# Kernel tuning notes

Hardware: AMD Instinct MI355X
Metric: run time of the kernel (lower is better)

Reference implementation:

```python
import jax, jax.numpy as jnp
import numpy as np

EPSILON = 1e-30

def compute_energy_density(F, lam, mu):
    # F: [E,3,3]; lam, mu: [E]
    C = jnp.einsum('...ji,...jk->...ik', F, F)
    J = jnp.linalg.det(F)
    Ic = C[..., 0, 0] + C[..., 1, 1] + C[..., 2, 2]
    delta = 1.0
    dim = 3
    alpha = (1.0 - 1.0 / (dim + delta)) * mu / lam + 1.0
    Ic_verified = jax.nn.relu(Ic + delta)
    return (mu / 2 * (Ic - dim)
            + lam / 2 * (J - alpha) ** 2
            - 0.5 * mu * jnp.log(Ic_verified + EPSILON))


def setup_inputs() -> dict:
    key = jax.random.key(0)
    ks = jax.random.split(key, 10)
    V, E = 8192, 40000
    next_position = jax.random.normal(ks[0], (V, 3), dtype=jnp.float32)
    position = jax.random.normal(ks[1], (V, 3), dtype=jnp.float32)
    velocity = jax.random.normal(ks[2], (V, 3), dtype=jnp.float32) * 0.1
    external_acceleration = jax.random.normal(ks[3], (V, 3), dtype=jnp.float32) * 0.1
    int_density_matrix = jax.random.uniform(ks[4], (V, V), dtype=jnp.float32)
    elements = jax.random.randint(ks[5], (E, 4), 0, V, dtype=jnp.int64)
    polynomials = jax.random.normal(ks[6], (E, 4, 4), dtype=jnp.float32)
    measure = jax.random.uniform(ks[7], (E, 4, 1), dtype=jnp.float32)
    lam = jax.random.uniform(ks[8], (E,), dtype=jnp.float32) + 1.0  # keep away from 0 (divided by in alpha)
    mu = jax.random.uniform(ks[9], (E,), dtype=jnp.float32) + 0.5
    time_step = jnp.ones((), dtype=jnp.float32)
    return {"next_position": next_position, "position": position, "velocity": velocity,
            "external_acceleration": external_acceleration, "int_density_matrix": int_density_matrix,
            "elements": elements, "polynomials": polynomials, "measure": measure,
            "lam": lam, "mu": mu, "time_step": time_step}


def reference(next_position, position, velocity, external_acceleration,
              int_density_matrix, elements, polynomials, measure, lam, mu, time_step):
    inv_h = 1.0 / time_step
    coefficient = inv_h ** 2 / 2
    # Kinetic term: einsum('ij,ji->', M, delta @ delta.T) == sum(delta * (M @ delta))
    # (avoids materializing the [V,V] delta @ delta.T intermediate)
    y = position + velocity * time_step + external_acceleration * time_step ** 2
    delta = next_position - y  # [V,3]
    kinetic_energy = coefficient * jnp.sum(delta * (int_density_matrix @ delta))
    # Elastic term: gather element vertex positions, build deformation gradient F
    basis_derivatives_q = polynomials[:, :4, :3]          # [E,4,3]
    local_position = next_position[elements]               # [E,4,3] gather
    F = jnp.einsum('bft,bfl->btl', local_position, basis_derivatives_q)  # [E,3,3]
    psi = compute_energy_density(F, lam, mu)               # [E]
    elastic_energy = jnp.einsum('b,b->', psi, measure[:, 3, 0])
    energy = kinetic_energy + elastic_energy
    return energy, kinetic_energy, elastic_energy
```

## Files before the change

kernel.cpp:

```cpp
#include <hip/hip_runtime.h>

#define V 8192
#define RPW 2
#define KBLOCKS (V / (RPW * 4))

__global__ __launch_bounds__(256) void prep_kernel(
    const float* __restrict__ next_pos, const float* __restrict__ pos,
    const float* __restrict__ vel, const float* __restrict__ ext,
    const float* __restrict__ dt_p, float* __restrict__ ws) {
  int i = blockIdx.x * blockDim.x + threadIdx.x;
  if (i < 2) ws[i] = 0.f;
  if (i < V) {
    float dt = dt_p[0];
    float dt2 = dt * dt;
    float* dx = ws + 16;
    float* dy = dx + V;
    float* dz = dy + V;
    dx[i] = next_pos[3*i+0] - (pos[3*i+0] + vel[3*i+0]*dt + ext[3*i+0]*dt2);
    dy[i] = next_pos[3*i+1] - (pos[3*i+1] + vel[3*i+1]*dt + ext[3*i+1]*dt2);
    dz[i] = next_pos[3*i+2] - (pos[3*i+2] + vel[3*i+2]*dt + ext[3*i+2]*dt2);
  }
}

__global__ __launch_bounds__(256) void kinetic_kernel(
    const float* __restrict__ M, const float* __restrict__ dsoa,
    float* __restrict__ acc) {
  const float* __restrict__ dx = dsoa;
  const float* __restrict__ dy = dsoa + V;
  const float* __restrict__ dz = dsoa + 2 * V;
  const float4* __restrict__ dx4 = (const float4*)dx;
  const float4* __restrict__ dy4 = (const float4*)dy;
  const float4* __restrict__ dz4 = (const float4*)dz;

  const int t = threadIdx.x;
  const int lane = t & 63;
  const int wv = t >> 6;
  const int wave = blockIdx.x * 4 + wv;
  const int r0 = wave * RPW;

  float rx[RPW], ry[RPW], rz[RPW];
#pragma unroll
  for (int r = 0; r < RPW; ++r) {
    rx[r] = dx[r0 + r];
    ry[r] = dy[r0 + r];
    rz[r] = dz[r0 + r];
  }

  float a = 0.f;
#pragma unroll 2
  for (int i = 0; i < V / 4 / 64; ++i) {
    const int k = i * 64 + lane;
    const float4 cx = dx4[k];
    const float4 cy = dy4[k];
    const float4 cz = dz4[k];
#pragma unroll
    for (int r = 0; r < RPW; ++r) {
      const float4 m = *(const float4*)(M + (size_t)(r0 + r) * V + 4 * k);
      a += m.x * (rx[r]*cx.x + ry[r]*cy.x + rz[r]*cz.x);
      a += m.y * (rx[r]*cx.y + ry[r]*cy.y + rz[r]*cz.y);
      a += m.z * (rx[r]*cx.z + ry[r]*cy.z + rz[r]*cz.z);
      a += m.w * (rx[r]*cx.w + ry[r]*cy.w + rz[r]*cz.w);
    }
  }

#pragma unroll
  for (int off = 32; off; off >>= 1) a += __shfl_down(a, off, 64);

  __shared__ float lds[4];
  if (lane == 0) lds[wv] = a;
  __syncthreads();
  if (t == 0) atomicAdd(acc, lds[0] + lds[1] + lds[2] + lds[3]);
}

__global__ __launch_bounds__(256) void elastic_kernel(
    const float* __restrict__ next_pos, const int* __restrict__ elements,
    const float* __restrict__ poly, const float* __restrict__ measure,
    const float* __restrict__ lam, const float* __restrict__ mu,
    float* __restrict__ acc, int E) {
  int e = blockIdx.x * blockDim.x + threadIdx.x;
  float contrib = 0.f;
  if (e < E) {
    float F00 = 0.f, F01 = 0.f, F02 = 0.f;
    float F10 = 0.f, F11 = 0.f, F12 = 0.f;
    float F20 = 0.f, F21 = 0.f, F22 = 0.f;
#pragma unroll
    for (int f = 0; f < 4; ++f) {
      int vi = elements[e * 4 + f];
      const float* p = next_pos + 3 * (size_t)vi;
      float px = p[0], py = p[1], pz = p[2];
      const float* b = poly + (size_t)e * 16 + f * 4;
      float b0 = b[0], b1 = b[1], b2 = b[2];
      F00 += px * b0; F01 += px * b1; F02 += px * b2;
      F10 += py * b0; F11 += py * b1; F12 += py * b2;
      F20 += pz * b0; F21 += pz * b1; F22 += pz * b2;
    }
    float Ic = F00*F00 + F01*F01 + F02*F02 +
               F10*F10 + F11*F11 + F12*F12 +
               F20*F20 + F21*F21 + F22*F22;
    float J = F00 * (F11 * F22 - F12 * F21)
            - F01 * (F10 * F22 - F12 * F20)
            + F02 * (F10 * F21 - F11 * F20);
    float l = lam[e], m = mu[e];
    float alpha = 0.75f * m / l + 1.f;
    float Icv = fmaxf(Ic + 1.f, 0.f);
    float d = J - alpha;
    float psi = 0.5f * m * (Ic - 3.f) + 0.5f * l * d * d
              - 0.5f * m * logf(Icv + 1e-30f);
    contrib = psi * measure[e * 4 + 3];
  }
#pragma unroll
  for (int off = 32; off; off >>= 1) contrib += __shfl_down(contrib, off, 64);
  __shared__ float w[4];
  int lane = threadIdx.x & 63, wv = threadIdx.x >> 6;
  if (lane == 0) w[wv] = contrib;
  __syncthreads();
  if (threadIdx.x == 0) atomicAdd(acc, w[0] + w[1] + w[2] + w[3]);
}

__global__ void finalize_kernel(const float* __restrict__ ws,
                                const float* __restrict__ dt_p,
                                float* __restrict__ out) {
  float dt = dt_p[0];
  float inv_h = 1.f / dt;
  float coeff = 0.5f * inv_h * inv_h;
  float kin = coeff * ws[0];
  float ela = ws[1];
  out[0] = kin + ela;
  out[1] = kin;
  out[2] = ela;
}

extern "C" void kernel_launch(void* const* d_in, const int* in_sizes, int n_in,
                              void* d_out, int out_size, void* d_ws, size_t ws_size,
                              hipStream_t stream) {
  const float* next_pos = (const float*)d_in[0];
  const float* pos      = (const float*)d_in[1];
  const float* vel      = (const float*)d_in[2];
  const float* ext      = (const float*)d_in[3];
  const float* M        = (const float*)d_in[4];
  const int*   elements = (const int*)d_in[5];
  const float* poly     = (const float*)d_in[6];
  const float* measure  = (const float*)d_in[7];
  const float* lam      = (const float*)d_in[8];
  const float* mu       = (const float*)d_in[9];
  const float* dt_p     = (const float*)d_in[10];
  float* out = (float*)d_out;
  float* ws  = (float*)d_ws;
  const int E = in_sizes[5] / 4;

  prep_kernel<<<(V + 255) / 256, 256, 0, stream>>>(next_pos, pos, vel, ext, dt_p, ws);
  kinetic_kernel<<<KBLOCKS, 256, 0, stream>>>(M, ws + 16, ws);
  elastic_kernel<<<(E + 255) / 256, 256, 0, stream>>>(next_pos, elements, poly,
                                                      measure, lam, mu, ws + 1, E);
  finalize_kernel<<<1, 1, 0, stream>>>(ws, dt_p, out);
}
```

Before: 388.5 us.

## Stage delta vectors in LDS tiles and batch M row loads per wave

The kinetic kernel now gives each wave a single row of M instead of two, which doubles the grid. The block cooperatively loads 1024-element tiles of the delta vectors into shared memory, so the vectors are no longer re-read from global or L2 by every wave. Each lane issues four float4 loads of M up front per tile to increase memory-level parallelism. In exchange the kernel adds two barriers per tile, halves per-wave work, and re-reads the vectors once per block, in a kernel that streams 256MB of M and is bandwidth-bound.

```diff
diff --git a/kernel.cpp b/kernel.cpp
--- a/kernel.cpp
+++ b/kernel.cpp
@@ -1,8 +1,10 @@
 #include <hip/hip_runtime.h>
 
 #define V 8192
-#define RPW 2
-#define KBLOCKS (V / (RPW * 4))
+#define TILE 1024
+#define NTILES (V / TILE)
+#define C4_PER_TILE (TILE / 4)
+#define ITERS (C4_PER_TILE / 64)
 
 __global__ __launch_bounds__(256) void prep_kernel(
     const float* __restrict__ next_pos, const float* __restrict__ pos,
@@ -25,51 +27,58 @@
 __global__ __launch_bounds__(256) void kinetic_kernel(
     const float* __restrict__ M, const float* __restrict__ dsoa,
     float* __restrict__ acc) {
-  const float* __restrict__ dx = dsoa;
-  const float* __restrict__ dy = dsoa + V;
-  const float* __restrict__ dz = dsoa + 2 * V;
-  const float4* __restrict__ dx4 = (const float4*)dx;
-  const float4* __restrict__ dy4 = (const float4*)dy;
-  const float4* __restrict__ dz4 = (const float4*)dz;
+  const float4* __restrict__ dx4 = (const float4*)dsoa;
+  const float4* __restrict__ dy4 = (const float4*)(dsoa + V);
+  const float4* __restrict__ dz4 = (const float4*)(dsoa + 2 * V);
+
+  __shared__ float4 lx[C4_PER_TILE], ly[C4_PER_TILE], lz[C4_PER_TILE];
+  __shared__ float wsum[4];
 
   const int t = threadIdx.x;
   const int lane = t & 63;
   const int wv = t >> 6;
-  const int wave = blockIdx.x * 4 + wv;
-  const int r0 = wave * RPW;
+  const int row = blockIdx.x * 4 + wv;
 
-  float rx[RPW], ry[RPW], rz[RPW];
-#pragma unroll
-  for (int r = 0; r < RPW; ++r) {
-    rx[r] = dx[r0 + r];
-    ry[r] = dy[r0 + r];
-    rz[r] = dz[r0 + r];
-  }
+  const float rx = ((const float*)dx4)[row];
+  const float ry = ((const float*)dy4)[row];
+  const float rz = ((const float*)dz4)[row];
+
+  const float4* __restrict__ Mrow4 = (const float4*)(M + (size_t)row * V);
 
   float a = 0.f;
-#pragma unroll 2
-  for (int i = 0; i < V / 4 / 64; ++i) {
-    const int k = i * 64 + lane;
-    const float4 cx = dx4[k];
-    const float4 cy = dy4[k];
-    const float4 cz = dz4[k];
+  for (int tl = 0; tl < NTILES; ++tl) {
+    const int g = tl * C4_PER_TILE + t;
+    lx[t] = dx4[g];
+    ly[t] = dy4[g];
+    lz[t] = dz4[g];
+    __syncthreads();
+
+    float4 mv[ITERS];
 #pragma unroll
-    for (int r = 0; r < RPW; ++r) {
-      const float4 m = *(const float4*)(M + (size_t)(r0 + r) * V + 4 * k);
-      a += m.x * (rx[r]*cx.x + ry[r]*cy.x + rz[r]*cz.x);
-      a += m.y * (rx[r]*cx.y + ry[r]*cy.y + rz[r]*cz.y);
-      a += m.z * (rx[r]*cx.z + ry[r]*cy.z + rz[r]*cz.z);
-      a += m.w * (rx[r]*cx.w + ry[r]*cy.w + rz[r]*cz.w);
+    for (int j = 0; j < ITERS; ++j)
+      mv[j] = Mrow4[tl * C4_PER_TILE + j * 64 + lane];
+
+#pragma unroll
+    for (int j = 0; j < ITERS; ++j) {
+      const int c = j * 64 + lane;
+      const float4 cx = lx[c];
+      const float4 cy = ly[c];
+      const float4 cz = lz[c];
+      const float4 m = mv[j];
+      a += m.x * (rx * cx.x + ry * cy.x + rz * cz.x);
+      a += m.y * (rx * cx.y + ry * cy.y + rz * cz.y);
+      a += m.z * (rx * cx.z + ry * cy.z + rz * cz.z);
+      a += m.w * (rx * cx.w + ry * cy.w + rz * cz.w);
     }
+    __syncthreads();
   }
 
 #pragma unroll
   for (int off = 32; off; off >>= 1) a += __shfl_down(a, off, 64);
 
-  __shared__ float lds[4];
-  if (lane == 0) lds[wv] = a;
+  if (lane == 0) wsum[wv] = a;
   __syncthreads();
-  if (t == 0) atomicAdd(acc, lds[0] + lds[1] + lds[2] + lds[3]);
+  if (t == 0) atomicAdd(acc, wsum[0] + wsum[1] + wsum[2] + wsum[3]);
 }
 
 __global__ __launch_bounds__(256) void elastic_kernel(
@@ -149,7 +158,7 @@
   const int E = in_sizes[5] / 4;
 
   prep_kernel<<<(V + 255) / 256, 256, 0, stream>>>(next_pos, pos, vel, ext, dt_p, ws);
-  kinetic_kernel<<<KBLOCKS, 256, 0, stream>>>(M, ws + 16, ws);
+  kinetic_kernel<<<V / 4, 256, 0, stream>>>(M, ws + 16, ws);
   elastic_kernel<<<(E + 255) / 256, 256, 0, stream>>>(next_pos, elements, poly,
                                                       measure, lam, mu, ws + 1, E);
   finalize_kernel<<<1, 1, 0, stream>>>(ws, dt_p, out);
```

New measurement: 411.3 us. 1.06x slower.

## Fuse prep with elastic, grid-stride kinetic GEMV, last-block finalize

Applied to the files above, without the earlier changes.

Merges the delta-prep and elastic-energy kernels into one launch, using block-index ranges to pick the role. The kinetic kernel now walks M as a flat float4 stream with a grid-stride pattern, each thread keeping one fixed column chunk of delta and re-reading row deltas from cache. The separate finalize kernel is replaced by a last-block-done atomic counter. This cuts launch count from four to two and aims for fully coalesced streaming of the 256MB matrix, at the cost of an extra atomic ticket and more scalar loads per iteration.

```diff
diff --git a/kernel.cpp b/kernel.cpp
--- a/kernel.cpp
+++ b/kernel.cpp
@@ -1,133 +1,154 @@
 #include <hip/hip_runtime.h>
 
 #define V 8192
-#define RPW 2
-#define KBLOCKS (V / (RPW * 4))
+#define PREP_BLOCKS 32
+#define KIN_BLOCKS 2048
+#define KIN_THREADS 256
+#define KIN_TOTAL (KIN_BLOCKS * KIN_THREADS)
 
-__global__ __launch_bounds__(256) void prep_kernel(
+
+__global__ __launch_bounds__(256) void prep_elastic_kernel(
     const float* __restrict__ next_pos, const float* __restrict__ pos,
     const float* __restrict__ vel, const float* __restrict__ ext,
-    const float* __restrict__ dt_p, float* __restrict__ ws) {
-  int i = blockIdx.x * blockDim.x + threadIdx.x;
-  if (i < 2) ws[i] = 0.f;
-  if (i < V) {
-    float dt = dt_p[0];
-    float dt2 = dt * dt;
+    const float* __restrict__ dt_p, const int* __restrict__ elements,
+    const float* __restrict__ poly, const float* __restrict__ measure,
+    const float* __restrict__ lam, const float* __restrict__ mu,
+    float* __restrict__ ws, int E) {
+  const int b = blockIdx.x;
+  const int t = threadIdx.x;
+
+  if (b < PREP_BLOCKS) {
+    if (b == 0 && t == 0) {
+      ws[0] = 0.f;
+      ((unsigned int*)ws)[2] = 0u;
+    }
+    const int i = b * 256 + t;
+    const float dt = dt_p[0];
+    const float dt2 = dt * dt;
     float* dx = ws + 16;
     float* dy = dx + V;
     float* dz = dy + V;
     dx[i] = next_pos[3*i+0] - (pos[3*i+0] + vel[3*i+0]*dt + ext[3*i+0]*dt2);
     dy[i] = next_pos[3*i+1] - (pos[3*i+1] + vel[3*i+1]*dt + ext[3*i+1]*dt2);
     dz[i] = next_pos[3*i+2] - (pos[3*i+2] + vel[3*i+2]*dt + ext[3*i+2]*dt2);
+  } else {
+    const int e = (b - PREP_BLOCKS) * 256 + t;
+    float contrib = 0.f;
+    if (e < E) {
+      float F00 = 0.f, F01 = 0.f, F02 = 0.f;
+      float F10 = 0.f, F11 = 0.f, F12 = 0.f;
+      float F20 = 0.f, F21 = 0.f, F22 = 0.f;
+#pragma unroll
+      for (int f = 0; f < 4; ++f) {
+        int vi = elements[e * 4 + f];
+        const float* p = next_pos + 3 * (size_t)vi;
+        float px = p[0], py = p[1], pz = p[2];
+        const float* bd = poly + (size_t)e * 16 + f * 4;
+        float b0 = bd[0], b1 = bd[1], b2 = bd[2];
+        F00 += px * b0; F01 += px * b1; F02 += px * b2;
+        F10 += py * b0; F11 += py * b1; F12 += py * b2;
+        F20 += pz * b0; F21 += pz * b1; F22 += pz * b2;
+      }
+      float Ic = F00*F00 + F01*F01 + F02*F02 +
+                 F10*F10 + F11*F11 + F12*F12 +
+                 F20*F20 + F21*F21 + F22*F22;
+      float J = F00 * (F11 * F22 - F12 * F21)
+              - F01 * (F10 * F22 - F12 * F20)
+              + F02 * (F10 * F21 - F11 * F20);
+      float l = lam[e], m = mu[e];
+      float alpha = 0.75f * m / l + 1.f;
+      float Icv = fmaxf(Ic + 1.f, 0.f);
+      float d = J - alpha;
+      float psi = 0.5f * m * (Ic - 3.f) + 0.5f * l * d * d
+                - 0.5f * m * logf(Icv + 1e-30f);
+      contrib = psi * measure[e * 4 + 3];
+    }
+#pragma unroll
+    for (int off = 32; off; off >>= 1) contrib += __shfl_down(contrib, off, 64);
+    __shared__ float w[4];
+    int lane = t & 63, wv = t >> 6;
+    if (lane == 0) w[wv] = contrib;
+    __syncthreads();
+    if (t == 0) atomicAdd(ws + 1, w[0] + w[1] + w[2] + w[3]);
   }
 }
 
-__global__ __launch_bounds__(256) void kinetic_kernel(
-    const float* __restrict__ M, const float* __restrict__ dsoa,
-    float* __restrict__ acc) {
-  const float* __restrict__ dx = dsoa;
-  const float* __restrict__ dy = dsoa + V;
-  const float* __restrict__ dz = dsoa + 2 * V;
-  const float4* __restrict__ dx4 = (const float4*)dx;
-  const float4* __restrict__ dy4 = (const float4*)dy;
-  const float4* __restrict__ dz4 = (const float4*)dz;
+__global__ __launch_bounds__(KIN_THREADS) void kinetic_kernel(
+    const float* __restrict__ M, float* __restrict__ ws,
+    const float* __restrict__ dt_p, float* __restrict__ out) {
+  const float* __restrict__ dsoa = ws + 16;
+  const float* __restrict__ dxs = dsoa;
+  const float* __restrict__ dys = dsoa + V;
+  const float* __restrict__ dzs = dsoa + 2 * V;
 
   const int t = threadIdx.x;
-  const int lane = t & 63;
-  const int wv = t >> 6;
-  const int wave = blockIdx.x * 4 + wv;
-  const int r0 = wave * RPW;
+  const unsigned base = blockIdx.x * KIN_THREADS + t;
 
-  float rx[RPW], ry[RPW], rz[RPW];
-#pragma unroll
-  for (int r = 0; r < RPW; ++r) {
-    rx[r] = dx[r0 + r];
-    ry[r] = dy[r0 + r];
-    rz[r] = dz[r0 + r];
-  }
+  const unsigned c = base & 2047u;
+  const float4 cx = ((const float4*)dxs)[c];
+  const float4 cy = ((const float4*)dys)[c];
+  const float4 cz = ((const float4*)dzs)[c];
+
+  const float4* __restrict__ M4 = (const float4*)M;
 
   float a = 0.f;
-#pragma unroll 2
-  for (int i = 0; i < V / 4 / 64; ++i) {
-    const int k = i * 64 + lane;
-    const float4 cx = dx4[k];
-    const float4 cy = dy4[k];
-    const float4 cz = dz4[k];
-#pragma unroll
-    for (int r = 0; r < RPW; ++r) {
-      const float4 m = *(const float4*)(M + (size_t)(r0 + r) * V + 4 * k);
-      a += m.x * (rx[r]*cx.x + ry[r]*cy.x + rz[r]*cz.x);
-      a += m.y * (rx[r]*cx.y + ry[r]*cy.y + rz[r]*cz.y);
-      a += m.z * (rx[r]*cx.z + ry[r]*cy.z + rz[r]*cz.z);
-      a += m.w * (rx[r]*cx.w + ry[r]*cy.w + rz[r]*cz.w);
-    }
+  const int NIT = (V / 4) * V / KIN_TOTAL;
+#pragma unroll 1
+  for (int it = 0; it < NIT; it += 4) {
+    unsigned g0 = base + (unsigned)(it + 0) * KIN_TOTAL;
+    unsigned g1 = base + (unsigned)(it + 1) * KIN_TOTAL;
+    unsigned g2 = base + (unsigned)(it + 2) * KIN_TOTAL;
+    unsigned g3 = base + (unsigned)(it + 3) * KIN_TOTAL;
+    float4 m0 = M4[g0];
+    float4 m1 = M4[g1];
+    float4 m2 = M4[g2];
+    float4 m3 = M4[g3];
+    unsigned r0 = g0 >> 11, r1 = g1 >> 11, r2 = g2 >> 11, r3 = g3 >> 11;
+    float rx0 = dxs[r0], ry0 = dys[r0], rz0 = dzs[r0];
+    float rx1 = dxs[r1], ry1 = dys[r1], rz1 = dzs[r1];
+    float rx2 = dxs[r2], ry2 = dys[r2], rz2 = dzs[r2];
+    float rx3 = dxs[r3], ry3 = dys[r3], rz3 = dzs[r3];
+    a += m0.x * (rx0*cx.x + ry0*cy.x + rz0*cz.x);
+    a += m0.y * (rx0*cx.y + ry0*cy.y + rz0*cz.y);
+    a += m0.z * (rx0*cx.z + ry0*cy.z + rz0*cz.z);
+    a += m0.w * (rx0*cx.w + ry0*cy.w + rz0*cz.w);
+    a += m1.x * (rx1*cx.x + ry1*cy.x + rz1*cz.x);
+    a += m1.y * (rx1*cx.y + ry1*cy.y + rz1*cz.y);
+    a += m1.z * (rx1*cx.z + ry1*cy.z + rz1*cz.z);
+    a += m1.w * (rx1*cx.w + ry1*cy.w + rz1*cz.w);
+    a += m2.x * (rx2*cx.x + ry2*cy.x + rz2*cz.x);
+    a += m2.y * (rx2*cx.y + ry2*cy.y + rz2*cz.y);
+    a += m2.z * (rx2*cx.z + ry2*cy.z + rz2*cz.z);
+    a += m2.w * (rx2*cx.w + ry2*cy.w + rz2*cz.w);
+    a += m3.x * (rx3*cx.x + ry3*cy.x + rz3*cz.x);
+    a += m3.y * (rx3*cx.y + ry3*cy.y + rz3*cz.y);
+    a += m3.z * (rx3*cx.z + ry3*cy.z + rz3*cz.z);
+    a += m3.w * (rx3*cx.w + ry3*cy.w + rz3*cz.w);
   }
 
 #pragma unroll
   for (int off = 32; off; off >>= 1) a += __shfl_down(a, off, 64);
+  __shared__ float w[4];
+  const int lane = t & 63, wv = t >> 6;
+  if (lane == 0) w[wv] = a;
+  __syncthreads();
 
-  __shared__ float lds[4];
-  if (lane == 0) lds[wv] = a;
-  __syncthreads();
-  if (t == 0) atomicAdd(acc, lds[0] + lds[1] + lds[2] + lds[3]);
-}
-
-__global__ __launch_bounds__(256) void elastic_kernel(
-    const float* __restrict__ next_pos, const int* __restrict__ elements,
-    const float* __restrict__ poly, const float* __restrict__ measure,
-    const float* __restrict__ lam, const float* __restrict__ mu,
-    float* __restrict__ acc, int E) {
-  int e = blockIdx.x * blockDim.x + threadIdx.x;
-  float contrib = 0.f;
-  if (e < E) {
-    float F00 = 0.f, F01 = 0.f, F02 = 0.f;
-    float F10 = 0.f, F11 = 0.f, F12 = 0.f;
-    float F20 = 0.f, F21 = 0.f, F22 = 0.f;
-#pragma unroll
-    for (int f = 0; f < 4; ++f) {
-      int vi = elements[e * 4 + f];
-      const float* p = next_pos + 3 * (size_t)vi;
-      float px = p[0], py = p[1], pz = p[2];
-      const float* b = poly + (size_t)e * 16 + f * 4;
-      float b0 = b[0], b1 = b[1], b2 = b[2];
-      F00 += px * b0; F01 += px * b1; F02 += px * b2;
-      F10 += py * b0; F11 += py * b1; F12 += py * b2;
-      F20 += pz * b0; F21 += pz * b1; F22 += pz * b2;
+  if (t == 0) {
+    atomicAdd(ws + 0, w[0] + w[1] + w[2] + w[3]);
+    __threadfence();
+    unsigned old = atomicAdd((unsigned int*)ws + 2, 1u);
+    if (old == KIN_BLOCKS - 1) {
+      __threadfence();
+      float raw = atomicAdd(ws + 0, 0.0f);
+      float ela = ws[1];
+      float dt = dt_p[0];
+      float inv_h = 1.f / dt;
+      float kin = 0.5f * inv_h * inv_h * raw;
+      out[0] = kin + ela;
+      out[1] = kin;
+      out[2] = ela;
     }
-    float Ic = F00*F00 + F01*F01 + F02*F02 +
-               F10*F10 + F11*F11 + F12*F12 +
-               F20*F20 + F21*F21 + F22*F22;
-    float J = F00 * (F11 * F22 - F12 * F21)
-            - F01 * (F10 * F22 - F12 * F20)
-            + F02 * (F10 * F21 - F11 * F20);
-    float l = lam[e], m = mu[e];
-    float alpha = 0.75f * m / l + 1.f;
-    float Icv = fmaxf(Ic + 1.f, 0.f);
-    float d = J - alpha;
-    float psi = 0.5f * m * (Ic - 3.f) + 0.5f * l * d * d
-              - 0.5f * m * logf(Icv + 1e-30f);
-    contrib = psi * measure[e * 4 + 3];
   }
-#pragma unroll
-  for (int off = 32; off; off >>= 1) contrib += __shfl_down(contrib, off, 64);
-  __shared__ float w[4];
-  int lane = threadIdx.x & 63, wv = threadIdx.x >> 6;
-  if (lane == 0) w[wv] = contrib;
-  __syncthreads();
-  if (threadIdx.x == 0) atomicAdd(acc, w[0] + w[1] + w[2] + w[3]);
-}
-
-__global__ void finalize_kernel(const float* __restrict__ ws,
-                                const float* __restrict__ dt_p,
-                                float* __restrict__ out) {
-  float dt = dt_p[0];
-  float inv_h = 1.f / dt;
-  float coeff = 0.5f * inv_h * inv_h;
-  float kin = coeff * ws[0];
-  float ela = ws[1];
-  out[0] = kin + ela;
-  out[1] = kin;
-  out[2] = ela;
 }
 
 extern "C" void kernel_launch(void* const* d_in, const int* in_sizes, int n_in,
@@ -148,9 +169,8 @@
   float* ws  = (float*)d_ws;
   const int E = in_sizes[5] / 4;
 
-  prep_kernel<<<(V + 255) / 256, 256, 0, stream>>>(next_pos, pos, vel, ext, dt_p, ws);
-  kinetic_kernel<<<KBLOCKS, 256, 0, stream>>>(M, ws + 16, ws);
-  elastic_kernel<<<(E + 255) / 256, 256, 0, stream>>>(next_pos, elements, poly,
-                                                      measure, lam, mu, ws + 1, E);
-  finalize_kernel<<<1, 1, 0, stream>>>(ws, dt_p, out);
+  const int eblocks = (E + 255) / 256;
+  prep_elastic_kernel<<<PREP_BLOCKS + eblocks, 256, 0, stream>>>(
+      next_pos, pos, vel, ext, dt_p, elements, poly, measure, lam, mu, ws, E);
+  kinetic_kernel<<<KIN_BLOCKS, KIN_THREADS, 0, stream>>>(M, ws, dt_p, out);
 }
```

Measured after the change: 474.8 us. 22.2% more time.
